# Performance work log

Hardware: AMD Instinct MI355X
Metric: run time of the kernel (lower is better)

## Reference

```python
import jax, jax.numpy as jnp
import numpy as np

N_NODES = 100_000
N_EDGES = 3_200_000
IN_CH = 128
HID = 64


def setup_inputs() -> dict:
    key = jax.random.key(0)
    k0, k1, k2, k3 = jax.random.split(key, 4)
    x = jax.random.normal(k0, (N_NODES, IN_CH), dtype=jnp.float32)
    edge_index = jax.random.randint(k1, (2, N_EDGES), 0, N_NODES)
    # GCNConv internal linear (no bias) -> W1; separate additive bias b1
    W1 = jax.random.normal(k2, (HID, IN_CH), dtype=jnp.float32) * 0.05
    b1 = jnp.zeros((HID,), dtype=jnp.float32)
    W2 = jax.random.normal(k3, (1, HID), dtype=jnp.float32) * 0.05
    b2 = jnp.zeros((1,), dtype=jnp.float32)
    return {"x": x, "edge_index": edge_index, "W1": W1, "b1": b1, "W2": W2, "b2": b2}


def reference(x, edge_index, W1, b1, W2, b2):
    n = x.shape[0]
    # --- GCNConv: add self-loops, symmetric degree normalization ---
    loops = jnp.arange(n, dtype=edge_index.dtype)
    src = jnp.concatenate([edge_index[0], loops])  # [E+N]
    dst = jnp.concatenate([edge_index[1], loops])  # [E+N]
    deg = jax.ops.segment_sum(jnp.ones_like(dst, dtype=x.dtype), dst, num_segments=n)
    dinv = jnp.where(deg > 0, jax.lax.rsqrt(deg), 0.0)
    norm = dinv[src] * dinv[dst]                   # [E+N]
    h = x @ W1.T                                   # [N, HID]
    msg = h[src] * norm[:, None]                   # [E+N, HID] gather
    agg = jax.ops.segment_sum(msg, dst, num_segments=n) + b1  # scatter-add
    # --- ReLU + Linear(hidden, 1) + squeeze ---
    out = jax.nn.relu(agg) @ W2.T + b2             # [N, 1]
    return out.squeeze(-1)
```

## Files before the change

### kernel.cpp

```cpp
#include <hip/hip_runtime.h>
#include <hip/hip_bf16.h>


typedef unsigned int u32;
typedef unsigned short u16;
typedef __attribute__((ext_vector_type(8))) short bf16x8;
typedef __attribute__((ext_vector_type(4))) float f32x4;

#define PK 4096
#define PTH 512
#define EPT (PK/PTH)
#define CAPB 9216

__device__ __forceinline__ short f2bf(float f) {
    __hip_bfloat16 h = __float2bfloat16(f);
    return *reinterpret_cast<short*>(&h);
}
__device__ __forceinline__ float bf2f(u16 u) {
    return __uint_as_float(((u32)u) << 16);
}
__device__ __forceinline__ bf16x8 pack8(float4 lo, float4 hi) {
    bf16x8 o;
    o[0] = f2bf(lo.x); o[1] = f2bf(lo.y); o[2] = f2bf(lo.z); o[3] = f2bf(lo.w);
    o[4] = f2bf(hi.x); o[5] = f2bf(hi.y); o[6] = f2bf(hi.z); o[7] = f2bf(hi.w);
    return o;
}

__global__ __launch_bounds__(512) void setup_kernel(int* __restrict__ bcnt,
                                                    const float* __restrict__ W1,
                                                    u16* __restrict__ wbf, int NB) {
    int t = threadIdx.x;
    if (blockIdx.x == 0) {
        if (t < NB) bcnt[t] = 0;
    } else {
#pragma unroll
        for (int i = 0; i < 16; ++i) wbf[i * 512 + t] = (u16)f2bf(W1[i * 512 + t]);
    }
}

__global__ __launch_bounds__(PTH) void part_kernel(const int* __restrict__ src,
                                                   const int* __restrict__ dst,
                                                   int* __restrict__ bcnt,
                                                   u32* __restrict__ ebuf, int E, int NB) {
    __shared__ u32 stage[PK];
    __shared__ u16 sbid[PK];
    __shared__ int h[512], loff[512], gbase[512], cur[512];
    int t = threadIdx.x;
    int e0 = blockIdx.x * PK;
    int e1 = e0 + PK; if (e1 > E) e1 = E;
    int cnt = e1 - e0;
    h[t] = 0; cur[t] = 0;
    __syncthreads();
    int dreg[EPT];
#pragma unroll
    for (int i = 0; i < EPT; ++i) {
        int e = e0 + i * PTH + t;
        dreg[i] = (e < e1) ? dst[e] : -1;
        if (dreg[i] >= 0) atomicAdd(&h[dreg[i] >> 8], 1);
    }
    __syncthreads();
    if (t < 64) {
        int carry = 0;
        for (int c = 0; c < 8; ++c) {
            int idx = c * 64 + t;
            int v = h[idx], incl = v;
            for (int d2 = 1; d2 < 64; d2 <<= 1) {
                int o = __shfl_up(incl, d2);
                if (t >= d2) incl += o;
            }
            loff[idx] = carry + incl - v;
            carry += __shfl(incl, 63);
        }
    }
    __syncthreads();
    if (t < NB) gbase[t] = t * CAPB + atomicAdd(&bcnt[t], h[t]);
    __syncthreads();
#pragma unroll
    for (int i = 0; i < EPT; ++i) {
        int d = dreg[i];
        if (d >= 0) {
            int e = e0 + i * PTH + t;
            int s = src[e];
            int bk = d >> 8;
            int r = atomicAdd(&cur[bk], 1);
            int p = loff[bk] + r;
            stage[p] = ((u32)(d & 255) << 17) | (u32)s;
            sbid[p] = (u16)bk;
        }
    }
    __syncthreads();
    for (int i = t; i < cnt; i += PTH) {
        int bk = sbid[i];
        ebuf[gbase[bk] + (i - loff[bk])] = stage[i];
    }
}

__global__ __launch_bounds__(512) void csrb2_kernel(const u32* __restrict__ ebuf,
                                                    const int* __restrict__ bcnt,
                                                    int* __restrict__ csr,
                                                    int* __restrict__ offs,
                                                    int* __restrict__ degc,
                                                    int N) {
    __shared__ u32 stage[CAPB];
    __shared__ int h2[256], lofs[256], cur2[256];
    int t = threadIdx.x;
    int b = blockIdx.x;
    int base = b << 8;
    int e0 = b * CAPB;
    int cnt = bcnt[b];
    if (t < 256) { h2[t] = 0; cur2[t] = 0; }
    __syncthreads();
    for (int e = t; e < cnt; e += 512) atomicAdd(&h2[(int)(ebuf[e0 + e] >> 17)], 1);
    __syncthreads();
    if (t < 64) {
        int carry = 0;
        for (int c = 0; c < 4; ++c) {
            int idx = c * 64 + t;
            int v = h2[idx], incl = v;
            for (int d2 = 1; d2 < 64; d2 <<= 1) {
                int o = __shfl_up(incl, d2);
                if (t >= d2) incl += o;
            }
            lofs[idx] = carry + incl - v;
            carry += __shfl(incl, 63);
        }
    }
    __syncthreads();
    if (t < 256) {
        int n = base + t;
        if (n < N) { offs[n] = e0 + lofs[t]; degc[n] = h2[t]; }
    }
    if (cnt <= CAPB) {
        for (int e = t; e < cnt; e += 512) {
            u32 pk = ebuf[e0 + e];
            int dl = (int)(pk >> 17);
            int r = atomicAdd(&cur2[dl], 1);
            stage[lofs[dl] + r] = pk & 0x1FFFF;
        }
        __syncthreads();
        for (int e = t; e < cnt; e += 512) csr[e0 + e] = (int)stage[e];
    } else {
        for (int e = t; e < cnt; e += 512) {
            u32 pk = ebuf[e0 + e];
            int dl = (int)(pk >> 17);
            int r = atomicAdd(&cur2[dl], 1);
            csr[e0 + lofs[dl] + r] = (int)(pk & 0x1FFFF);
        }
    }
}

__global__ __launch_bounds__(256) void gemm_kernel(const float* __restrict__ x,
                                                   const u16* __restrict__ wbf,
                                                   const int* __restrict__ degc,
                                                   u16* __restrict__ gb, int N) {
    int t = threadIdx.x;
    int lane = t & 63;
    int wv = t >> 6;
    int n0 = blockIdx.x * 64 + wv * 16;
    int r = lane & 15;
    int g = lane >> 4;

    int nr = n0 + r; if (nr >= N) nr = N - 1;
    const float* xrow = x + (size_t)nr * 128 + g * 8;
    bf16x8 afr[4];
#pragma unroll
    for (int ks = 0; ks < 4; ++ks) {
        float4 lo = *(const float4*)(xrow + ks * 32);
        float4 hi = *(const float4*)(xrow + ks * 32 + 4);
        afr[ks] = pack8(lo, hi);
    }

    f32x4 acc[4] = {f32x4{0.f,0.f,0.f,0.f}, f32x4{0.f,0.f,0.f,0.f},
                    f32x4{0.f,0.f,0.f,0.f}, f32x4{0.f,0.f,0.f,0.f}};
#pragma unroll
    for (int ct = 0; ct < 4; ++ct) {
        const u16* wrow = wbf + (ct * 16 + r) * 128 + g * 8;
#pragma unroll
        for (int ks = 0; ks < 4; ++ks) {
            bf16x8 bfr = *(const bf16x8*)(wrow + ks * 32);
            acc[ct] = __builtin_amdgcn_mfma_f32_16x16x32_bf16(afr[ks], bfr, acc[ct], 0, 0, 0);
        }
    }

#pragma unroll
    for (int reg = 0; reg < 4; ++reg) {
        int n = n0 + g * 4 + reg;
        if (n < N) {
            float dv = rsqrtf((float)(degc[n] + 1));
#pragma unroll
            for (int ct = 0; ct < 4; ++ct)
                gb[(size_t)n * 64 + ct * 16 + r] = (u16)f2bf(dv * acc[ct][reg]);
        }
    }
}

__global__ __launch_bounds__(256) void agg_kernel(const u16* __restrict__ gb,
                                                  const int* __restrict__ csr,
                                                  const int* __restrict__ offs,
                                                  const int* __restrict__ degc,
                                                  const float* __restrict__ W2,
                                                  const float* __restrict__ b1,
                                                  const float* __restrict__ b2,
                                                  float* __restrict__ out, int N) {
    int wid = blockIdx.x * 4 + (threadIdx.x >> 6);
    int lane = threadIdx.x & 63;
    if (wid >= N) return;
    int off = __builtin_amdgcn_readfirstlane(offs[wid]);
    int cnt = __builtin_amdgcn_readfirstlane(degc[wid]);
    const u16* gbl = gb + lane;
    float acc = bf2f(gbl[(size_t)wid * 64]);
    int j = 0;
    for (; j + 32 <= cnt; j += 32) {
        float v[32];
#pragma unroll
        for (int k = 0; k < 32; ++k) {
            int s = csr[off + j + k];
            v[k] = bf2f(gbl[(size_t)s * 64]);
        }
        float p0 = ((v[0]+v[1])+(v[2]+v[3])) + ((v[4]+v[5])+(v[6]+v[7]));
        float p1 = ((v[8]+v[9])+(v[10]+v[11])) + ((v[12]+v[13])+(v[14]+v[15]));
        float p2 = ((v[16]+v[17])+(v[18]+v[19])) + ((v[20]+v[21])+(v[22]+v[23]));
        float p3 = ((v[24]+v[25])+(v[26]+v[27])) + ((v[28]+v[29])+(v[30]+v[31]));
        acc += (p0 + p1) + (p2 + p3);
    }
    for (; j + 16 <= cnt; j += 16) {
        float v[16];
#pragma unroll
        for (int k = 0; k < 16; ++k) {
            int s = csr[off + j + k];
            v[k] = bf2f(gbl[(size_t)s * 64]);
        }
        float p0 = ((v[0]+v[1])+(v[2]+v[3])) + ((v[4]+v[5])+(v[6]+v[7]));
        float p1 = ((v[8]+v[9])+(v[10]+v[11])) + ((v[12]+v[13])+(v[14]+v[15]));
        acc += p0 + p1;
    }
    for (; j + 4 <= cnt; j += 4) {
        float v[4];
#pragma unroll
        for (int k = 0; k < 4; ++k) {
            int s = csr[off + j + k];
            v[k] = bf2f(gbl[(size_t)s * 64]);
        }
        acc += (v[0] + v[1]) + (v[2] + v[3]);
    }
    for (; j < cnt; ++j) {
        int s = csr[off + j];
        acc += bf2f(gbl[(size_t)s * 64]);
    }
    float dv = rsqrtf((float)(cnt + 1));
    float val = fmaxf(dv * acc + b1[lane], 0.f) * W2[lane];
#pragma unroll
    for (int o = 32; o >= 1; o >>= 1) val += __shfl_xor(val, o);
    if (lane == 0) out[wid] = val + b2[0];
}

extern "C" void kernel_launch(void* const* d_in, const int* in_sizes, int n_in,
                              void* d_out, int out_size, void* d_ws, size_t ws_size,
                              hipStream_t stream) {
    const float* x  = (const float*)d_in[0];
    const int*   ei = (const int*)d_in[1];
    const float* W1 = (const float*)d_in[2];
    const float* b1 = (const float*)d_in[3];
    const float* W2 = (const float*)d_in[4];
    const float* b2 = (const float*)d_in[5];
    float* out = (float*)d_out;

    int N = in_sizes[0] / 128;
    int E = in_sizes[1] / 2;
    const int* src = ei;
    const int* dst = ei + E;
    int NB = (N + 255) >> 8;
    int NBLK = (E + PK - 1) / PK;

    char* ws = (char*)d_ws;
    int* bcnt = (int*)(ws + 0x000000);
    int* degc = (int*)(ws + 0x010000);
    int* offs = (int*)(ws + 0x080000);
    u16* wbf  = (u16*)(ws + 0x0F0000);
    u32* ebuf = (u32*)(ws + 0x100000);
    u16* gb   = (u16*)(ws + 0x100000);
    int* csr  = (int*)(ws + 0xF80000);

    setup_kernel<<<2, 512, 0, stream>>>(bcnt, W1, wbf, NB);
    part_kernel<<<NBLK, PTH, 0, stream>>>(src, dst, bcnt, ebuf, E, NB);
    csrb2_kernel<<<NB, 512, 0, stream>>>(ebuf, bcnt, csr, offs, degc, N);
    gemm_kernel<<<(N + 63) / 64, 256, 0, stream>>>(x, wbf, degc, gb, N);
    agg_kernel<<<(N + 3) / 4, 256, 0, stream>>>(gb, csr, offs, degc, W2, b1, b2, out, N);
}
```

Measured before the change: 135.5 us.

## Fuse GEMM into CSR build kernel, sort edges in place, stagger bucket atomics

Merges the dense x@W1 MFMA GEMM into the per-bucket CSR kernel, so each 256-node block computes its scaled hidden rows using the degree histogram already in shared memory. This removes one kernel launch and the global degc read. The sorted sources are written back into ebuf in place instead of a separate csr array, and the overflow path is dropped by clamping cnt to CAPB. The partition kernel now staggers its per-bucket atomicAdd order by block index to reduce contention, and the aggregation kernel drops its 32-wide unrolled loop. The clamp silently loses edges if a bucket ever exceeds capacity.

```diff
diff --git a/kernel.cpp b/kernel.cpp
--- a/kernel.cpp
+++ b/kernel.cpp
@@ -73,7 +73,11 @@
         }
     }
     __syncthreads();
-    if (t < NB) gbase[t] = t * CAPB + atomicAdd(&bcnt[t], h[t]);
+    if (t < NB) {
+        int bb = t + (blockIdx.x % NB);
+        if (bb >= NB) bb -= NB;
+        gbase[bb] = bb * CAPB + atomicAdd(&bcnt[bb], h[bb]);
+    }
     __syncthreads();
 #pragma unroll
     for (int i = 0; i < EPT; ++i) {
@@ -95,12 +99,14 @@
     }
 }
 
-__global__ __launch_bounds__(512) void csrb2_kernel(const u32* __restrict__ ebuf,
-                                                    const int* __restrict__ bcnt,
-                                                    int* __restrict__ csr,
-                                                    int* __restrict__ offs,
-                                                    int* __restrict__ degc,
-                                                    int N) {
+__global__ __launch_bounds__(512) void csrg_kernel(u32* ebuf,
+                                                   const int* __restrict__ bcnt,
+                                                   int* __restrict__ offs,
+                                                   int* __restrict__ degc,
+                                                   const float* __restrict__ x,
+                                                   const u16* __restrict__ wbf,
+                                                   u16* __restrict__ gb,
+                                                   int N) {
     __shared__ u32 stage[CAPB];
     __shared__ int h2[256], lofs[256], cur2[256];
     int t = threadIdx.x;
@@ -108,6 +114,7 @@
     int base = b << 8;
     int e0 = b * CAPB;
     int cnt = bcnt[b];
+    if (cnt > CAPB) cnt = CAPB;
     if (t < 256) { h2[t] = 0; cur2[t] = 0; }
     __syncthreads();
     for (int e = t; e < cnt; e += 512) atomicAdd(&h2[(int)(ebuf[e0 + e] >> 17)], 1);
@@ -130,68 +137,55 @@
         int n = base + t;
         if (n < N) { offs[n] = e0 + lofs[t]; degc[n] = h2[t]; }
     }
-    if (cnt <= CAPB) {
-        for (int e = t; e < cnt; e += 512) {
-            u32 pk = ebuf[e0 + e];
-            int dl = (int)(pk >> 17);
-            int r = atomicAdd(&cur2[dl], 1);
-            stage[lofs[dl] + r] = pk & 0x1FFFF;
-        }
-        __syncthreads();
-        for (int e = t; e < cnt; e += 512) csr[e0 + e] = (int)stage[e];
-    } else {
-        for (int e = t; e < cnt; e += 512) {
-            u32 pk = ebuf[e0 + e];
-            int dl = (int)(pk >> 17);
-            int r = atomicAdd(&cur2[dl], 1);
-            csr[e0 + lofs[dl] + r] = (int)(pk & 0x1FFFF);
-        }
-    }
-}
-
-__global__ __launch_bounds__(256) void gemm_kernel(const float* __restrict__ x,
-                                                   const u16* __restrict__ wbf,
-                                                   const int* __restrict__ degc,
-                                                   u16* __restrict__ gb, int N) {
-    int t = threadIdx.x;
+
     int lane = t & 63;
     int wv = t >> 6;
-    int n0 = blockIdx.x * 64 + wv * 16;
     int r = lane & 15;
     int g = lane >> 4;
-
-    int nr = n0 + r; if (nr >= N) nr = N - 1;
-    const float* xrow = x + (size_t)nr * 128 + g * 8;
-    bf16x8 afr[4];
-#pragma unroll
-    for (int ks = 0; ks < 4; ++ks) {
-        float4 lo = *(const float4*)(xrow + ks * 32);
-        float4 hi = *(const float4*)(xrow + ks * 32 + 4);
-        afr[ks] = pack8(lo, hi);
-    }
-
-    f32x4 acc[4] = {f32x4{0.f,0.f,0.f,0.f}, f32x4{0.f,0.f,0.f,0.f},
-                    f32x4{0.f,0.f,0.f,0.f}, f32x4{0.f,0.f,0.f,0.f}};
-#pragma unroll
-    for (int ct = 0; ct < 4; ++ct) {
-        const u16* wrow = wbf + (ct * 16 + r) * 128 + g * 8;
+#pragma unroll
+    for (int it = 0; it < 2; ++it) {
+        int n0 = base + (it * 8 + wv) * 16;
+        int nr = n0 + r; if (nr >= N) nr = N - 1;
+        const float* xrow = x + (size_t)nr * 128 + g * 8;
+        bf16x8 afr[4];
 #pragma unroll
         for (int ks = 0; ks < 4; ++ks) {
-            bf16x8 bfr = *(const bf16x8*)(wrow + ks * 32);
-            acc[ct] = __builtin_amdgcn_mfma_f32_16x16x32_bf16(afr[ks], bfr, acc[ct], 0, 0, 0);
-        }
-    }
-
-#pragma unroll
-    for (int reg = 0; reg < 4; ++reg) {
-        int n = n0 + g * 4 + reg;
-        if (n < N) {
-            float dv = rsqrtf((float)(degc[n] + 1));
-#pragma unroll
-            for (int ct = 0; ct < 4; ++ct)
-                gb[(size_t)n * 64 + ct * 16 + r] = (u16)f2bf(dv * acc[ct][reg]);
-        }
-    }
+            float4 lo = *(const float4*)(xrow + ks * 32);
+            float4 hi = *(const float4*)(xrow + ks * 32 + 4);
+            afr[ks] = pack8(lo, hi);
+        }
+        f32x4 acc[4] = {f32x4{0.f,0.f,0.f,0.f}, f32x4{0.f,0.f,0.f,0.f},
+                        f32x4{0.f,0.f,0.f,0.f}, f32x4{0.f,0.f,0.f,0.f}};
+#pragma unroll
+        for (int ct = 0; ct < 4; ++ct) {
+            const u16* wrow = wbf + (ct * 16 + r) * 128 + g * 8;
+#pragma unroll
+            for (int ks = 0; ks < 4; ++ks) {
+                bf16x8 bfr = *(const bf16x8*)(wrow + ks * 32);
+                acc[ct] = __builtin_amdgcn_mfma_f32_16x16x32_bf16(afr[ks], bfr, acc[ct], 0, 0, 0);
+            }
+        }
+#pragma unroll
+        for (int reg = 0; reg < 4; ++reg) {
+            int n = n0 + g * 4 + reg;
+            if (n < N) {
+                int dl = n - base;
+                float dv = rsqrtf((float)(h2[dl] + 1));
+#pragma unroll
+                for (int ct = 0; ct < 4; ++ct)
+                    gb[(size_t)n * 64 + ct * 16 + r] = (u16)f2bf(dv * acc[ct][reg]);
+            }
+        }
+    }
+
+    for (int e = t; e < cnt; e += 512) {
+        u32 pk = ebuf[e0 + e];
+        int dl = (int)(pk >> 17);
+        int rr = atomicAdd(&cur2[dl], 1);
+        stage[lofs[dl] + rr] = pk & 0x1FFFF;
+    }
+    __syncthreads();
+    for (int e = t; e < cnt; e += 512) ebuf[e0 + e] = stage[e];
 }
 
 __global__ __launch_bounds__(256) void agg_kernel(const u16* __restrict__ gb,
@@ -210,19 +204,6 @@
     const u16* gbl = gb + lane;
     float acc = bf2f(gbl[(size_t)wid * 64]);
     int j = 0;
-    for (; j + 32 <= cnt; j += 32) {
-        float v[32];
-#pragma unroll
-        for (int k = 0; k < 32; ++k) {
-            int s = csr[off + j + k];
-            v[k] = bf2f(gbl[(size_t)s * 64]);
-        }
-        float p0 = ((v[0]+v[1])+(v[2]+v[3])) + ((v[4]+v[5])+(v[6]+v[7]));
-        float p1 = ((v[8]+v[9])+(v[10]+v[11])) + ((v[12]+v[13])+(v[14]+v[15]));
-        float p2 = ((v[16]+v[17])+(v[18]+v[19])) + ((v[20]+v[21])+(v[22]+v[23]));
-        float p3 = ((v[24]+v[25])+(v[26]+v[27])) + ((v[28]+v[29])+(v[30]+v[31]));
-        acc += (p0 + p1) + (p2 + p3);
-    }
     for (; j + 16 <= cnt; j += 16) {
         float v[16];
 #pragma unroll
@@ -230,9 +211,11 @@
             int s = csr[off + j + k];
             v[k] = bf2f(gbl[(size_t)s * 64]);
         }
-        float p0 = ((v[0]+v[1])+(v[2]+v[3])) + ((v[4]+v[5])+(v[6]+v[7]));
-        float p1 = ((v[8]+v[9])+(v[10]+v[11])) + ((v[12]+v[13])+(v[14]+v[15]));
-        acc += p0 + p1;
+        float s01 = (v[0] + v[1]) + (v[2] + v[3]);
+        float s23 = (v[4] + v[5]) + (v[6] + v[7]);
+        float s45 = (v[8] + v[9]) + (v[10] + v[11]);
+        float s67 = (v[12] + v[13]) + (v[14] + v[15]);
+        acc += (s01 + s23) + (s45 + s67);
     }
     for (; j + 4 <= cnt; j += 4) {
         float v[4];
@@ -278,12 +261,10 @@
     int* offs = (int*)(ws + 0x080000);
     u16* wbf  = (u16*)(ws + 0x0F0000);
     u32* ebuf = (u32*)(ws + 0x100000);
-    u16* gb   = (u16*)(ws + 0x100000);
-    int* csr  = (int*)(ws + 0xF80000);
+    u16* gb   = (u16*)(ws + 0xF80000);
 
     setup_kernel<<<2, 512, 0, stream>>>(bcnt, W1, wbf, NB);
     part_kernel<<<NBLK, PTH, 0, stream>>>(src, dst, bcnt, ebuf, E, NB);
-    csrb2_kernel<<<NB, 512, 0, stream>>>(ebuf, bcnt, csr, offs, degc, N);
-    gemm_kernel<<<(N + 63) / 64, 256, 0, stream>>>(x, wbf, degc, gb, N);
-    agg_kernel<<<(N + 3) / 4, 256, 0, stream>>>(gb, csr, offs, degc, W2, b1, b2, out, N);
-}
+    csrg_kernel<<<NB, 512, 0, stream>>>(ebuf, bcnt, offs, degc, x, wbf, gb, N);
+    agg_kernel<<<(N + 3) / 4, 256, 0, stream>>>(gb, (const int*)ebuf, offs, degc, W2, b1, b2, out, N);
+}
```

Measured after the change: 135.7 us. Within noise of the previous version (+0.1%).
